# Optimization experiments

Measured on AMD Instinct MI355X. Metric: run time of the kernel, lower is better.

## Reference

```python
import jax, jax.numpy as jnp
import numpy as np

N, E, F_IN, D, R, L = 50000, 800000, 128, 64, 8, 3


def setup_inputs() -> dict:
    key = jax.random.key(0)
    ks = jax.random.split(key, 8)
    x = jax.random.normal(ks[0], (N, F_IN), dtype=jnp.float32)
    edge_index = jax.random.randint(ks[1], (2, E), 0, N)
    dist = jax.random.uniform(ks[2], (E,), dtype=jnp.float32)
    etype = jax.random.randint(ks[3], (E,), 0, R).astype(jnp.float32)
    edge_attr = jnp.stack([dist, etype], axis=1)  # [E, 2]: col0 distance, col1 relation id
    W_in = jax.random.normal(ks[4], (F_IN, D), dtype=jnp.float32) / np.float32(np.sqrt(F_IN))
    b_in = jnp.zeros((D,), jnp.float32)
    W_rel = jax.random.normal(ks[5], (L, R, D, D), dtype=jnp.float32) / np.float32(np.sqrt(D))
    W_root = jax.random.normal(ks[6], (L, D, D), dtype=jnp.float32) / np.float32(np.sqrt(D))
    b_conv = jnp.zeros((L, D), jnp.float32)
    return dict(x=x, edge_index=edge_index, edge_attr=edge_attr, W_in=W_in,
                b_in=b_in, W_rel=W_rel, W_root=W_root, b_conv=b_conv)


def rgcn_conv(h, src, dst, etype, Wr, Wroot, b):
    # PyG RGCNConv: per-relation MEAN aggregation + root weight + bias.
    # Composite segment id (dst, relation) -> one scatter over N*R segments.
    seg = dst * R + etype  # [E]
    msg = h[src]  # [E, D] gather
    s = jax.ops.segment_sum(msg, seg, num_segments=N * R)            # [N*R, D]
    cnt = jax.ops.segment_sum(jnp.ones((E,), h.dtype), seg, num_segments=N * R)
    mean = (s / jnp.maximum(cnt, 1.0)[:, None]).reshape(N, R, D)     # [N, R, D]
    return jnp.einsum('nrd,rde->ne', mean, Wr) + h @ Wroot + b


def reference(x, edge_index, edge_attr, W_in, b_in, W_rel, W_root, b_conv):
    edge_type = edge_attr[:, 1].astype(jnp.int32)
    edge_distance = edge_attr[:, 0]
    src, dst = edge_index[0], edge_index[1]
    h = jax.nn.relu(x @ W_in + b_in)
    for l in range(L):
        h = jax.nn.relu(rgcn_conv(h, src, dst, edge_type, W_rel[l], W_root[l], b_conv[l]))
    return h, edge_distance
```

## Files before the change

### kernel.cpp

```cpp
#include <hip/hip_runtime.h>

#define NN 50000
#define EE 800000
#define FIN 128
#define DD 64
#define RR 8
#define LL 3

#define ND (NN*DD)
#define NR (NN*RR)

#define SB 1024
#define NSB ((NR + SB - 1) / SB)
#define ECAP 2048
#define AS 72
#define KB 576

typedef __attribute__((ext_vector_type(8))) short bf16x8;
typedef __attribute__((ext_vector_type(4))) float f32x4;

__device__ __forceinline__ unsigned short f2bf(float x) {
  unsigned u = __float_as_uint(x);
  u += 0x7fff + ((u >> 16) & 1);
  return (unsigned short)(u >> 16);
}
__device__ __forceinline__ void split_bf(float x, short& h, short& l) {
  unsigned short hu = f2bf(x);
  float hf = __uint_as_float((unsigned)hu << 16);
  h = (short)hu;
  l = (short)f2bf(x - hf);
}

__global__ void k_prepB(const float* __restrict__ W_rel,
                        const float* __restrict__ W_root,
                        short* __restrict__ Btp) {
  const int idx = blockIdx.x * 256 + threadIdx.x;
  if (idx >= LL * DD * KB) return;
  const int k = idx % KB, n = (idx / KB) % DD, l = idx / (KB * DD);
  float w;
  if (k < 512) w = W_rel[(((size_t)l*RR + (k >> 6))*DD + (k & 63))*DD + n];
  else         w = W_root[((size_t)l*DD + (k - 512))*DD + n];
  short hi, lo; split_bf(w, hi, lo);
  Btp[((size_t)(l*2+0)*DD + n)*KB + k] = hi;
  Btp[((size_t)(l*2+1)*DD + n)*KB + k] = lo;
}
__global__ void k_prepWin(const float* __restrict__ W_in, short* __restrict__ Wt) {
  const int idx = blockIdx.x * 256 + threadIdx.x;
  if (idx >= DD * FIN) return;
  const int k = idx % FIN, n = idx / FIN;
  float w = W_in[(size_t)k*DD + n];
  short hi, lo; split_bf(w, hi, lo);
  Wt[((size_t)0*DD + n)*FIN + k] = hi;
  Wt[((size_t)1*DD + n)*FIN + k] = lo;
}

__global__ __launch_bounds__(256) void k_input_mfma(
    const float* __restrict__ x, const short* __restrict__ Wt,
    const float* __restrict__ b, float* __restrict__ h) {
  __shared__ short Ah[DD * 136];
  __shared__ short Al[DD * 136];
  const int t = threadIdx.x;
  const int lane = t & 63, wv = t >> 6;
  const int lr = lane & 15, lc = lane >> 4;
  const int n0 = blockIdx.x * 64;

  {
    const int row = t >> 2, cb = (t & 3) * 32;
    const int n = n0 + row;
    #pragma unroll
    for (int i = 0; i < 8; ++i) {
      const int col = cb + i * 4;
      float4 v = make_float4(0.f,0.f,0.f,0.f);
      if (n < NN) v = *(const float4*)(x + (size_t)n*FIN + col);
      short h0,l0,h1,l1,h2,l2,h3,l3;
      split_bf(v.x,h0,l0); split_bf(v.y,h1,l1);
      split_bf(v.z,h2,l2); split_bf(v.w,h3,l3);
      unsigned long long ph = (unsigned short)h0 | ((unsigned long long)(unsigned short)h1<<16)
          | ((unsigned long long)(unsigned short)h2<<32) | ((unsigned long long)(unsigned short)h3<<48);
      unsigned long long pl = (unsigned short)l0 | ((unsigned long long)(unsigned short)l1<<16)
          | ((unsigned long long)(unsigned short)l2<<32) | ((unsigned long long)(unsigned short)l3<<48);
      *(unsigned long long*)&Ah[row*136 + col] = ph;
      *(unsigned long long*)&Al[row*136 + col] = pl;
    }
  }
  __syncthreads();

  const int m0 = wv * 16;
  f32x4 acc[4];
  #pragma unroll
  for (int nt = 0; nt < 4; ++nt) acc[nt] = (f32x4){0.f,0.f,0.f,0.f};
  const int aoff = (m0 + lr)*136 + lc*8;
  int boff[4];
  #pragma unroll
  for (int nt = 0; nt < 4; ++nt) boff[nt] = (nt*16 + lr)*FIN + lc*8;

  #pragma unroll
  for (int ks = 0; ks < 4; ++ks) {
    const bf16x8 ah = *(const bf16x8*)&Ah[aoff + ks*32];
    const bf16x8 al = *(const bf16x8*)&Al[aoff + ks*32];
    #pragma unroll
    for (int nt = 0; nt < 4; ++nt) {
      const bf16x8 bh = *(const bf16x8*)(Wt + boff[nt] + ks*32);
      const bf16x8 bl = *(const bf16x8*)(Wt + DD*FIN + boff[nt] + ks*32);
      acc[nt] = __builtin_amdgcn_mfma_f32_16x16x32_bf16(ah, bh, acc[nt], 0, 0, 0);
      acc[nt] = __builtin_amdgcn_mfma_f32_16x16x32_bf16(al, bh, acc[nt], 0, 0, 0);
      acc[nt] = __builtin_amdgcn_mfma_f32_16x16x32_bf16(ah, bl, acc[nt], 0, 0, 0);
    }
  }
  #pragma unroll
  for (int nt = 0; nt < 4; ++nt) {
    const float bb = b[nt*16 + lr];
    #pragma unroll
    for (int i = 0; i < 4; ++i) {
      const int m = n0 + m0 + lc*4 + i;
      if (m < NN) h[(size_t)m*DD + nt*16 + lr] = fmaxf(acc[nt][i] + bb, 0.f);
    }
  }
}

__global__ void k_hist(const int* __restrict__ ei, const float* __restrict__ ea,
                       int* __restrict__ rp) {
  const int e = blockIdx.x * 256 + threadIdx.x;
  if (e >= EE) return;
  atomicAdd(&rp[(int)ea[2*e + 1] * NN + ei[EE + e]], 1);
}

__global__ __launch_bounds__(256) void k_scan1(int* __restrict__ rp,
                                               int* __restrict__ part) {
  __shared__ int ls[256];
  const int t = threadIdx.x;
  const int base = blockIdx.x * SB + t * 4;
  int v[4] = {0,0,0,0};
  #pragma unroll
  for (int i = 0; i < 4; ++i)
    if (base + i < NR) v[i] = rp[base + i];
  const int tsum = v[0] + v[1] + v[2] + v[3];
  ls[t] = tsum; __syncthreads();
  #pragma unroll
  for (int off = 1; off < 256; off <<= 1) {
    int x = (t >= off) ? ls[t - off] : 0;
    __syncthreads();
    ls[t] += x;
    __syncthreads();
  }
  if (t == 255) part[blockIdx.x] = ls[255];
  int run = ls[t] - tsum;
  #pragma unroll
  for (int i = 0; i < 4; ++i) {
    if (base + i < NR) rp[base + i] = run;
    run += v[i];
  }
}

__global__ __launch_bounds__(512) void k_scan2(int* __restrict__ part) {
  __shared__ int ls[512];
  const int t = threadIdx.x;
  const int v = (t < NSB) ? part[t] : 0;
  ls[t] = v; __syncthreads();
  #pragma unroll
  for (int off = 1; off < 512; off <<= 1) {
    int x = (t >= off) ? ls[t - off] : 0;
    __syncthreads();
    ls[t] += x;
    __syncthreads();
  }
  if (t < NSB) part[t] = ls[t] - v;
}

__global__ __launch_bounds__(256) void k_scan3(int* __restrict__ rp,
                                               const int* __restrict__ part,
                                               int* __restrict__ fill) {
  const int base = blockIdx.x * SB + threadIdx.x * 4;
  const int off = part[blockIdx.x];
  #pragma unroll
  for (int i = 0; i < 4; ++i)
    if (base + i < NR) {
      const int r = rp[base + i] + off;
      rp[base + i] = r;
      fill[base + i] = r;
    }
  if (blockIdx.x == 0 && threadIdx.x == 0) rp[NR] = EE;
}

__global__ void k_reorder(const int* __restrict__ ei, const float* __restrict__ ea,
                          int* __restrict__ fill, unsigned short* __restrict__ eidx) {
  const int e = blockIdx.x * 256 + threadIdx.x;
  if (e >= EE) return;
  const int key = (int)ea[2*e + 1] * NN + ei[EE + e];
  const int pos = atomicAdd(&fill[key], 1);
  eidx[pos] = (unsigned short)ei[e];
}

__global__ __launch_bounds__(256) void k_layer(
    const float* __restrict__ h, const unsigned short* __restrict__ eidx,
    const int* __restrict__ rp, const short* __restrict__ Btp,
    const float* __restrict__ bias, float* __restrict__ outh) {
  __shared__ short Ah[DD * AS];
  __shared__ short Al[DD * AS];
  __shared__ unsigned short els[ECAP];
  __shared__ int rpls[RR][65];
  __shared__ int baseL[RR + 1];

  const int t = threadIdx.x;
  const int lane = t & 63, wv = t >> 6;
  const int lr = lane & 15, lc = lane >> 4;
  const int n0 = blockIdx.x * 64;
  const int j0 = wv * 16;
  const float* hl = h + lane;

  for (int i = t; i < RR * 65; i += 256) {
    const int kk = i / 65, j = i - kk * 65;
    int g = n0 + j; if (g > NN) g = NN;
    rpls[kk][j] = rp[kk * NN + g];
  }
  __syncthreads();
  if (t == 0) {
    int s = 0;
    #pragma unroll
    for (int k = 0; k < RR; ++k) { baseL[k] = s; s += rpls[k][64] - rpls[k][0]; }
    baseL[RR] = s;
  }
  __syncthreads();
  const bool fit = baseL[RR] <= ECAP;
  if (fit) {
    for (int k = 0; k < RR; ++k) {
      const int g0 = rpls[k][0], sp = rpls[k][64] - g0, b0 = baseL[k];
      for (int i = t; i < sp; i += 256) els[b0 + i] = eidx[g0 + i];
    }
  }
  __syncthreads();

  auto gather = [&](int kk) {
    const int ebeg = rpls[kk][j0], eend = rpls[kk][j0 + 16];
    int j = j0;
    int nxt = rpls[kk][j0 + 1];
    float acc = 0.f;
    auto flush = [&]() {
      const int cnt = nxt - rpls[kk][j];
      float m = (cnt > 1) ? acc * (1.0f / (float)cnt) : acc;
      short hb, lb; split_bf(m, hb, lb);
      Ah[j * AS + lane] = hb;
      Al[j * AS + lane] = lb;
    };
    auto proc = [&](float v, int e2) {
      while (e2 >= nxt) { flush(); acc = 0.f; ++j; nxt = rpls[kk][j + 1]; }
      acc += v;
    };
    auto scan = [&](auto srcAt) {
      int e = ebeg;
      for (; e + 15 < eend; e += 16) {
        int s[16]; float v[16];
        #pragma unroll
        for (int i = 0; i < 16; ++i) s[i] = srcAt(e + i);
        #pragma unroll
        for (int i = 0; i < 16; ++i) v[i] = hl[(size_t)s[i] * DD];
        #pragma unroll
        for (int i = 0; i < 16; ++i) proc(v[i], e + i);
      }
      if (e + 7 < eend) {
        int s[8]; float v[8];
        #pragma unroll
        for (int i = 0; i < 8; ++i) s[i] = srcAt(e + i);
        #pragma unroll
        for (int i = 0; i < 8; ++i) v[i] = hl[(size_t)s[i] * DD];
        #pragma unroll
        for (int i = 0; i < 8; ++i) proc(v[i], e + i);
        e += 8;
      }
      for (; e < eend; ++e) proc(hl[(size_t)srcAt(e) * DD], e);
    };
    if (fit) {
      const int lb2 = baseL[kk] - rpls[kk][0];
      scan([&](int e) { return (int)els[lb2 + e]; });
    } else {
      scan([&](int e) { return (int)eidx[e]; });
    }
    while (true) {
      flush();
      acc = 0.f; ++j;
      if (j >= j0 + 16) break;
      nxt = rpls[kk][j + 1];
    }
  };
  auto root_stage = [&]() {
    for (int jj = 0; jj < 16; jj += 4) {
      float v[4];
      #pragma unroll
      for (int i = 0; i < 4; ++i) {
        const int n = n0 + j0 + jj + i;
        v[i] = (n < NN) ? h[(size_t)n * DD + lane] : 0.f;
      }
      #pragma unroll
      for (int i = 0; i < 4; ++i) {
        short hb, lb; split_bf(v[i], hb, lb);
        Ah[(j0 + jj + i) * AS + lane] = hb;
        Al[(j0 + jj + i) * AS + lane] = lb;
      }
    }
  };

  const int m0 = wv * 16;
  f32x4 acc[4];
  #pragma unroll
  for (int nt = 0; nt < 4; ++nt) acc[nt] = (f32x4){0.f,0.f,0.f,0.f};
  const int aoff = (m0 + lr) * AS + lc * 8;
  int boff[4];
  #pragma unroll
  for (int nt = 0; nt < 4; ++nt) boff[nt] = (nt*16 + lr)*KB + lc*8;
  const short* Blo = Btp + (size_t)DD * KB;

  #pragma unroll 1
  for (int kk = 0; kk < 9; ++kk) {
    if (kk < 8) gather(kk);
    else        root_stage();
    const int koff = kk * 64;
    #pragma unroll
    for (int ks = 0; ks < 2; ++ks) {
      const bf16x8 ah = *(const bf16x8*)&Ah[aoff + ks*32];
      const bf16x8 al = *(const bf16x8*)&Al[aoff + ks*32];
      #pragma unroll
      for (int nt = 0; nt < 4; ++nt) {
        const bf16x8 bh = *(const bf16x8*)(Btp + boff[nt] + koff + ks*32);
        const bf16x8 bl = *(const bf16x8*)(Blo + boff[nt] + koff + ks*32);
        acc[nt] = __builtin_amdgcn_mfma_f32_16x16x32_bf16(ah, bh, acc[nt], 0, 0, 0);
        acc[nt] = __builtin_amdgcn_mfma_f32_16x16x32_bf16(al, bh, acc[nt], 0, 0, 0);
        acc[nt] = __builtin_amdgcn_mfma_f32_16x16x32_bf16(ah, bl, acc[nt], 0, 0, 0);
      }
    }
  }

  #pragma unroll
  for (int nt = 0; nt < 4; ++nt) {
    const float bb = bias[nt*16 + lr];
    #pragma unroll
    for (int i = 0; i < 4; ++i) {
      const int m = n0 + m0 + lc*4 + i;
      if (m < NN) outh[(size_t)m*DD + nt*16 + lr] = fmaxf(acc[nt][i] + bb, 0.f);
    }
  }
}

__global__ void k_edist(const float* __restrict__ ea, float* __restrict__ out) {
  const int e = blockIdx.x * 256 + threadIdx.x;
  if (e < EE) out[e] = ea[2*e];
}

extern "C" void kernel_launch(void* const* d_in, const int* in_sizes, int n_in,
                              void* d_out, int out_size, void* d_ws, size_t ws_size,
                              hipStream_t stream) {
  const float* x      = (const float*)d_in[0];
  const int*   ei     = (const int*)d_in[1];
  const float* ea     = (const float*)d_in[2];
  const float* W_in   = (const float*)d_in[3];
  const float* b_in   = (const float*)d_in[4];
  const float* W_rel  = (const float*)d_in[5];
  const float* W_root = (const float*)d_in[6];
  const float* b_conv = (const float*)d_in[7];
  float* out = (float*)d_out;

  char* ws = (char*)d_ws;
  float*          hA   = (float*)(ws);
  float*          hB   = (float*)(ws + 12800000);
  int*            rp   = (int*)  (ws + 25600000);
  int*            fill = (int*)  (ws + 27200256);
  unsigned short* eidx = (unsigned short*)(ws + 28800256);
  int*            part = (int*)  (ws + 30400256);
  short*          Btp  = (short*)(ws + 30402304);
  short*          Wt   = (short*)(ws + 30844672);

  k_edist<<<(EE + 255)/256, 256, 0, stream>>>(ea, out + (size_t)ND);
  k_prepB<<<(LL*DD*KB + 255)/256, 256, 0, stream>>>(W_rel, W_root, Btp);
  k_prepWin<<<(DD*FIN + 255)/256, 256, 0, stream>>>(W_in, Wt);
  k_input_mfma<<<(NN + 63)/64, 256, 0, stream>>>(x, Wt, b_in, hA);

  hipMemsetAsync(rp, 0, (size_t)NR*4, stream);
  k_hist<<<(EE + 255)/256, 256, 0, stream>>>(ei, ea, rp);
  k_scan1<<<NSB, 256, 0, stream>>>(rp, part);
  k_scan2<<<1, 512, 0, stream>>>(part);
  k_scan3<<<NSB, 256, 0, stream>>>(rp, part, fill);
  k_reorder<<<(EE + 255)/256, 256, 0, stream>>>(ei, ea, fill, eidx);

  const int NBL = (NN + 63) / 64;
  const float* hin = hA;
  for (int l = 0; l < LL; ++l) {
    float* hout = (l == 2) ? out : ((l == 0) ? hB : hA);
    k_layer<<<NBL, 256, 0, stream>>>(hin, eidx, rp,
        Btp + (size_t)l*2*DD*KB, b_conv + (size_t)l*DD, hout);
    hin = hout;
  }
}
```

Measured before the change: 403.7 us.

## Software-pipeline edge gathers across relations and fuse small prep kernels

After: 796.6 us. 97.3% more time.

```diff
diff --git a/kernel.cpp b/kernel.cpp
--- a/kernel.cpp
+++ b/kernel.cpp
@@ -31,27 +31,27 @@
   l = (short)f2bf(x - hf);
 }
 
-__global__ void k_prepB(const float* __restrict__ W_rel,
-                        const float* __restrict__ W_root,
-                        short* __restrict__ Btp) {
+__global__ void k_prep(const float* __restrict__ W_rel,
+                       const float* __restrict__ W_root,
+                       const float* __restrict__ W_in,
+                       short* __restrict__ Btp, short* __restrict__ Wt) {
   const int idx = blockIdx.x * 256 + threadIdx.x;
-  if (idx >= LL * DD * KB) return;
-  const int k = idx % KB, n = (idx / KB) % DD, l = idx / (KB * DD);
-  float w;
-  if (k < 512) w = W_rel[(((size_t)l*RR + (k >> 6))*DD + (k & 63))*DD + n];
-  else         w = W_root[((size_t)l*DD + (k - 512))*DD + n];
-  short hi, lo; split_bf(w, hi, lo);
-  Btp[((size_t)(l*2+0)*DD + n)*KB + k] = hi;
-  Btp[((size_t)(l*2+1)*DD + n)*KB + k] = lo;
-}
-__global__ void k_prepWin(const float* __restrict__ W_in, short* __restrict__ Wt) {
-  const int idx = blockIdx.x * 256 + threadIdx.x;
-  if (idx >= DD * FIN) return;
-  const int k = idx % FIN, n = idx / FIN;
-  float w = W_in[(size_t)k*DD + n];
-  short hi, lo; split_bf(w, hi, lo);
-  Wt[((size_t)0*DD + n)*FIN + k] = hi;
-  Wt[((size_t)1*DD + n)*FIN + k] = lo;
+  if (idx < LL * DD * KB) {
+    const int k = idx % KB, n = (idx / KB) % DD, l = idx / (KB * DD);
+    float w;
+    if (k < 512) w = W_rel[(((size_t)l*RR + (k >> 6))*DD + (k & 63))*DD + n];
+    else         w = W_root[((size_t)l*DD + (k - 512))*DD + n];
+    short hi, lo; split_bf(w, hi, lo);
+    Btp[((size_t)(l*2+0)*DD + n)*KB + k] = hi;
+    Btp[((size_t)(l*2+1)*DD + n)*KB + k] = lo;
+  }
+  if (idx < DD * FIN) {
+    const int k = idx % FIN, n = idx / FIN;
+    float w = W_in[(size_t)k*DD + n];
+    short hi, lo; split_bf(w, hi, lo);
+    Wt[((size_t)0*DD + n)*FIN + k] = hi;
+    Wt[((size_t)1*DD + n)*FIN + k] = lo;
+  }
 }
 
 __global__ __launch_bounds__(256) void k_input_mfma(
@@ -119,10 +119,12 @@
 }
 
 __global__ void k_hist(const int* __restrict__ ei, const float* __restrict__ ea,
-                       int* __restrict__ rp) {
+                       int* __restrict__ rp, float* __restrict__ outd) {
   const int e = blockIdx.x * 256 + threadIdx.x;
   if (e >= EE) return;
-  atomicAdd(&rp[(int)ea[2*e + 1] * NN + ei[EE + e]], 1);
+  const float2 v = *(const float2*)(ea + 2*e);
+  outd[e] = v.x;
+  atomicAdd(&rp[(int)v.y * NN + ei[EE + e]], 1);
 }
 
 __global__ __launch_bounds__(256) void k_scan1(int* __restrict__ rp,
@@ -230,50 +232,71 @@
   }
   __syncthreads();
 
-  auto gather = [&](int kk) {
-    const int ebeg = rpls[kk][j0], eend = rpls[kk][j0 + 16];
-    int j = j0;
-    int nxt = rpls[kk][j0 + 1];
+  float va[16], vb[16];
+  auto issue16 = [&](float (&v)[16], int base, int ee1, int lb) {
+    #pragma unroll
+    for (int i = 0; i < 16; ++i) {
+      int idx = base + i;
+      idx = (idx < ee1) ? idx : ee1;
+      const int s = fit ? (int)els[lb + idx] : (int)eidx[idx];
+      v[i] = hl[(size_t)s * DD];
+    }
+  };
+
+  const int m0 = wv * 16;
+  f32x4 acc4[4];
+  #pragma unroll
+  for (int nt = 0; nt < 4; ++nt) acc4[nt] = (f32x4){0.f,0.f,0.f,0.f};
+  const int aoff = (m0 + lr) * AS + lc * 8;
+  int boff[4];
+  #pragma unroll
+  for (int nt = 0; nt < 4; ++nt) boff[nt] = (nt*16 + lr)*KB + lc*8;
+  const short* Blo = Btp + (size_t)DD * KB;
+
+  {
+    const int eb = rpls[0][j0], ee = rpls[0][j0 + 16];
+    const int lb = fit ? (baseL[0] - rpls[0][0]) : 0;
+    if (eb < ee) {
+      issue16(va, eb, ee - 1, lb);
+      if (eb + 16 < ee) issue16(vb, eb + 16, ee - 1, lb);
+    }
+  }
+
+  #pragma unroll 1
+  for (int kk = 0; kk < 8; ++kk) {
+    const int eb = rpls[kk][j0], ee = rpls[kk][j0 + 16];
+    const int lb = fit ? (baseL[kk] - rpls[kk][0]) : 0;
+    int j = j0, nxt = rpls[kk][j0 + 1];
     float acc = 0.f;
     auto flush = [&]() {
       const int cnt = nxt - rpls[kk][j];
       float m = (cnt > 1) ? acc * (1.0f / (float)cnt) : acc;
-      short hb, lb; split_bf(m, hb, lb);
+      short hb, lbv; split_bf(m, hb, lbv);
       Ah[j * AS + lane] = hb;
-      Al[j * AS + lane] = lb;
+      Al[j * AS + lane] = lbv;
     };
     auto proc = [&](float v, int e2) {
       while (e2 >= nxt) { flush(); acc = 0.f; ++j; nxt = rpls[kk][j + 1]; }
       acc += v;
     };
-    auto scan = [&](auto srcAt) {
-      int e = ebeg;
-      for (; e + 15 < eend; e += 16) {
-        int s[16]; float v[16];
-        #pragma unroll
-        for (int i = 0; i < 16; ++i) s[i] = srcAt(e + i);
-        #pragma unroll
-        for (int i = 0; i < 16; ++i) v[i] = hl[(size_t)s[i] * DD];
-        #pragma unroll
-        for (int i = 0; i < 16; ++i) proc(v[i], e + i);
+    auto procB = [&](float (&v)[16], int base) {
+      #pragma unroll
+      for (int i = 0; i < 16; ++i)
+        if (base + i < ee) proc(v[i], base + i);
+    };
+
+    if (eb < ee) {
+      int base = eb;
+      while (true) {
+        if (base + 16 >= ee) { procB(va, base); break; }
+        procB(va, base);
+        if (base + 32 < ee) issue16(va, base + 32, ee - 1, lb);
+        base += 16;
+        if (base + 16 >= ee) { procB(vb, base); break; }
+        procB(vb, base);
+        if (base + 32 < ee) issue16(vb, base + 32, ee - 1, lb);
+        base += 16;
       }
-      if (e + 7 < eend) {
-        int s[8]; float v[8];
-        #pragma unroll
-        for (int i = 0; i < 8; ++i) s[i] = srcAt(e + i);
-        #pragma unroll
-        for (int i = 0; i < 8; ++i) v[i] = hl[(size_t)s[i] * DD];
-        #pragma unroll
-        for (int i = 0; i < 8; ++i) proc(v[i], e + i);
-        e += 8;
-      }
-      for (; e < eend; ++e) proc(hl[(size_t)srcAt(e) * DD], e);
-    };
-    if (fit) {
-      const int lb2 = baseL[kk] - rpls[kk][0];
-      scan([&](int e) { return (int)els[lb2 + e]; });
-    } else {
-      scan([&](int e) { return (int)eidx[e]; });
     }
     while (true) {
       flush();
@@ -281,38 +304,22 @@
       if (j >= j0 + 16) break;
       nxt = rpls[kk][j + 1];
     }
-  };
-  auto root_stage = [&]() {
-    for (int jj = 0; jj < 16; jj += 4) {
-      float v[4];
+
+    if (kk < 7) {
+      const int eb2 = rpls[kk + 1][j0], ee2 = rpls[kk + 1][j0 + 16];
+      const int lbn = fit ? (baseL[kk + 1] - rpls[kk + 1][0]) : 0;
+      if (eb2 < ee2) {
+        issue16(va, eb2, ee2 - 1, lbn);
+        if (eb2 + 16 < ee2) issue16(vb, eb2 + 16, ee2 - 1, lbn);
+      }
+    } else {
       #pragma unroll
-      for (int i = 0; i < 4; ++i) {
-        const int n = n0 + j0 + jj + i;
-        v[i] = (n < NN) ? h[(size_t)n * DD + lane] : 0.f;
+      for (int i = 0; i < 16; ++i) {
+        const int n = n0 + j0 + i;
+        va[i] = (n < NN) ? h[(size_t)n * DD + lane] : 0.f;
       }
-      #pragma unroll
-      for (int i = 0; i < 4; ++i) {
-        short hb, lb; split_bf(v[i], hb, lb);
-        Ah[(j0 + jj + i) * AS + lane] = hb;
-        Al[(j0 + jj + i) * AS + lane] = lb;
-      }
-    }
-  };
-
-  const int m0 = wv * 16;
-  f32x4 acc[4];
-  #pragma unroll
-  for (int nt = 0; nt < 4; ++nt) acc[nt] = (f32x4){0.f,0.f,0.f,0.f};
-  const int aoff = (m0 + lr) * AS + lc * 8;
-  int boff[4];
-  #pragma unroll
-  for (int nt = 0; nt < 4; ++nt) boff[nt] = (nt*16 + lr)*KB + lc*8;
-  const short* Blo = Btp + (size_t)DD * KB;
-
-  #pragma unroll 1
-  for (int kk = 0; kk < 9; ++kk) {
-    if (kk < 8) gather(kk);
-    else        root_stage();
+    }
+
     const int koff = kk * 64;
     #pragma unroll
     for (int ks = 0; ks < 2; ++ks) {
@@ -322,9 +329,32 @@
       for (int nt = 0; nt < 4; ++nt) {
         const bf16x8 bh = *(const bf16x8*)(Btp + boff[nt] + koff + ks*32);
         const bf16x8 bl = *(const bf16x8*)(Blo + boff[nt] + koff + ks*32);
-        acc[nt] = __builtin_amdgcn_mfma_f32_16x16x32_bf16(ah, bh, acc[nt], 0, 0, 0);
-        acc[nt] = __builtin_amdgcn_mfma_f32_16x16x32_bf16(al, bh, acc[nt], 0, 0, 0);
-        acc[nt] = __builtin_amdgcn_mfma_f32_16x16x32_bf16(ah, bl, acc[nt], 0, 0, 0);
+        acc4[nt] = __builtin_amdgcn_mfma_f32_16x16x32_bf16(ah, bh, acc4[nt], 0, 0, 0);
+        acc4[nt] = __builtin_amdgcn_mfma_f32_16x16x32_bf16(al, bh, acc4[nt], 0, 0, 0);
+        acc4[nt] = __builtin_amdgcn_mfma_f32_16x16x32_bf16(ah, bl, acc4[nt], 0, 0, 0);
+      }
+    }
+  }
+
+  #pragma unroll
+  for (int i = 0; i < 16; ++i) {
+    short hb, lbv; split_bf(va[i], hb, lbv);
+    Ah[(j0 + i) * AS + lane] = hb;
+    Al[(j0 + i) * AS + lane] = lbv;
+  }
+  {
+    const int koff = 512;
+    #pragma unroll
+    for (int ks = 0; ks < 2; ++ks) {
+      const bf16x8 ah = *(const bf16x8*)&Ah[aoff + ks*32];
+      const bf16x8 al = *(const bf16x8*)&Al[aoff + ks*32];
+      #pragma unroll
+      for (int nt = 0; nt < 4; ++nt) {
+        const bf16x8 bh = *(const bf16x8*)(Btp + boff[nt] + koff + ks*32);
+        const bf16x8 bl = *(const bf16x8*)(Blo + boff[nt] + koff + ks*32);
+        acc4[nt] = __builtin_amdgcn_mfma_f32_16x16x32_bf16(ah, bh, acc4[nt], 0, 0, 0);
+        acc4[nt] = __builtin_amdgcn_mfma_f32_16x16x32_bf16(al, bh, acc4[nt], 0, 0, 0);
+        acc4[nt] = __builtin_amdgcn_mfma_f32_16x16x32_bf16(ah, bl, acc4[nt], 0, 0, 0);
       }
     }
   }
@@ -335,14 +365,9 @@
     #pragma unroll
     for (int i = 0; i < 4; ++i) {
       const int m = n0 + m0 + lc*4 + i;
-      if (m < NN) outh[(size_t)m*DD + nt*16 + lr] = fmaxf(acc[nt][i] + bb, 0.f);
-    }
-  }
-}
-
-__global__ void k_edist(const float* __restrict__ ea, float* __restrict__ out) {
-  const int e = blockIdx.x * 256 + threadIdx.x;
-  if (e < EE) out[e] = ea[2*e];
+      if (m < NN) outh[(size_t)m*DD + nt*16 + lr] = fmaxf(acc4[nt][i] + bb, 0.f);
+    }
+  }
 }
 
 extern "C" void kernel_launch(void* const* d_in, const int* in_sizes, int n_in,
@@ -368,13 +393,11 @@
   short*          Btp  = (short*)(ws + 30402304);
   short*          Wt   = (short*)(ws + 30844672);
 
-  k_edist<<<(EE + 255)/256, 256, 0, stream>>>(ea, out + (size_t)ND);
-  k_prepB<<<(LL*DD*KB + 255)/256, 256, 0, stream>>>(W_rel, W_root, Btp);
-  k_prepWin<<<(DD*FIN + 255)/256, 256, 0, stream>>>(W_in, Wt);
+  k_prep<<<(LL*DD*KB + 255)/256, 256, 0, stream>>>(W_rel, W_root, W_in, Btp, Wt);
   k_input_mfma<<<(NN + 63)/64, 256, 0, stream>>>(x, Wt, b_in, hA);
 
   hipMemsetAsync(rp, 0, (size_t)NR*4, stream);
-  k_hist<<<(EE + 255)/256, 256, 0, stream>>>(ei, ea, rp);
+  k_hist<<<(EE + 255)/256, 256, 0, stream>>>(ei, ea, rp, out + (size_t)ND);
   k_scan1<<<NSB, 256, 0, stream>>>(rp, part);
   k_scan2<<<1, 512, 0, stream>>>(part);
   k_scan3<<<NSB, 256, 0, stream>>>(rp, part, fill);
```

## Split relation gather across wave pairs with split-K reduction in layer kernel

Applied to the files above, without the earlier changes.

New measurement: 455.3 us. +12.8%, slower.

```diff
diff --git a/kernel.cpp b/kernel.cpp
--- a/kernel.cpp
+++ b/kernel.cpp
@@ -12,8 +12,8 @@
 
 #define SB 1024
 #define NSB ((NR + SB - 1) / SB)
-#define ECAP 2048
-#define AS 72
+#define ECAP 1024
+#define ASF 68
 #define KB 576
 
 typedef __attribute__((ext_vector_type(8))) short bf16x8;
@@ -31,27 +31,27 @@
   l = (short)f2bf(x - hf);
 }
 
-__global__ void k_prepB(const float* __restrict__ W_rel,
-                        const float* __restrict__ W_root,
-                        short* __restrict__ Btp) {
+__global__ void k_prep(const float* __restrict__ W_rel,
+                       const float* __restrict__ W_root,
+                       const float* __restrict__ W_in,
+                       short* __restrict__ Btp, short* __restrict__ Wt) {
   const int idx = blockIdx.x * 256 + threadIdx.x;
-  if (idx >= LL * DD * KB) return;
-  const int k = idx % KB, n = (idx / KB) % DD, l = idx / (KB * DD);
-  float w;
-  if (k < 512) w = W_rel[(((size_t)l*RR + (k >> 6))*DD + (k & 63))*DD + n];
-  else         w = W_root[((size_t)l*DD + (k - 512))*DD + n];
-  short hi, lo; split_bf(w, hi, lo);
-  Btp[((size_t)(l*2+0)*DD + n)*KB + k] = hi;
-  Btp[((size_t)(l*2+1)*DD + n)*KB + k] = lo;
-}
-__global__ void k_prepWin(const float* __restrict__ W_in, short* __restrict__ Wt) {
-  const int idx = blockIdx.x * 256 + threadIdx.x;
-  if (idx >= DD * FIN) return;
-  const int k = idx % FIN, n = idx / FIN;
-  float w = W_in[(size_t)k*DD + n];
-  short hi, lo; split_bf(w, hi, lo);
-  Wt[((size_t)0*DD + n)*FIN + k] = hi;
-  Wt[((size_t)1*DD + n)*FIN + k] = lo;
+  if (idx < LL * DD * KB) {
+    const int k = idx % KB, n = (idx / KB) % DD, l = idx / (KB * DD);
+    float w;
+    if (k < 512) w = W_rel[(((size_t)l*RR + (k >> 6))*DD + (k & 63))*DD + n];
+    else         w = W_root[((size_t)l*DD + (k - 512))*DD + n];
+    short hi, lo; split_bf(w, hi, lo);
+    Btp[((size_t)(l*2+0)*DD + n)*KB + k] = hi;
+    Btp[((size_t)(l*2+1)*DD + n)*KB + k] = lo;
+  }
+  if (idx < DD * FIN) {
+    const int k = idx % FIN, n = idx / FIN;
+    float w = W_in[(size_t)k*DD + n];
+    short hi, lo; split_bf(w, hi, lo);
+    Wt[((size_t)0*DD + n)*FIN + k] = hi;
+    Wt[((size_t)1*DD + n)*FIN + k] = lo;
+  }
 }
 
 __global__ __launch_bounds__(256) void k_input_mfma(
@@ -119,10 +119,12 @@
 }
 
 __global__ void k_hist(const int* __restrict__ ei, const float* __restrict__ ea,
-                       int* __restrict__ rp) {
+                       int* __restrict__ rp, float* __restrict__ outd) {
   const int e = blockIdx.x * 256 + threadIdx.x;
   if (e >= EE) return;
-  atomicAdd(&rp[(int)ea[2*e + 1] * NN + ei[EE + e]], 1);
+  const float2 v = *(const float2*)(ea + 2*e);
+  outd[e] = v.x;
+  atomicAdd(&rp[(int)v.y * NN + ei[EE + e]], 1);
 }
 
 __global__ __launch_bounds__(256) void k_scan1(int* __restrict__ rp,
@@ -191,25 +193,25 @@
   eidx[pos] = (unsigned short)ei[e];
 }
 
-__global__ __launch_bounds__(256) void k_layer(
+__global__ __launch_bounds__(256, 6) void k_layer(
     const float* __restrict__ h, const unsigned short* __restrict__ eidx,
     const int* __restrict__ rp, const short* __restrict__ Btp,
     const float* __restrict__ bias, float* __restrict__ outh) {
-  __shared__ short Ah[DD * AS];
-  __shared__ short Al[DD * AS];
+  __shared__ float Af[4][16 * ASF];
   __shared__ unsigned short els[ECAP];
-  __shared__ int rpls[RR][65];
+  __shared__ int rpls[RR][33];
   __shared__ int baseL[RR + 1];
 
   const int t = threadIdx.x;
   const int lane = t & 63, wv = t >> 6;
+  const int pair = wv >> 1, half = wv & 1;
   const int lr = lane & 15, lc = lane >> 4;
-  const int n0 = blockIdx.x * 64;
-  const int j0 = wv * 16;
+  const int n0 = blockIdx.x * 32;
+  const int j0 = pair * 16;
   const float* hl = h + lane;
 
-  for (int i = t; i < RR * 65; i += 256) {
-    const int kk = i / 65, j = i - kk * 65;
+  for (int i = t; i < RR * 33; i += 256) {
+    const int kk = i / 33, j = i - kk * 33;
     int g = n0 + j; if (g > NN) g = NN;
     rpls[kk][j] = rp[kk * NN + g];
   }
@@ -217,18 +219,20 @@
   if (t == 0) {
     int s = 0;
     #pragma unroll
-    for (int k = 0; k < RR; ++k) { baseL[k] = s; s += rpls[k][64] - rpls[k][0]; }
+    for (int k = 0; k < RR; ++k) { baseL[k] = s; s += rpls[k][32] - rpls[k][0]; }
     baseL[RR] = s;
   }
   __syncthreads();
   const bool fit = baseL[RR] <= ECAP;
   if (fit) {
     for (int k = 0; k < RR; ++k) {
-      const int g0 = rpls[k][0], sp = rpls[k][64] - g0, b0 = baseL[k];
+      const int g0 = rpls[k][0], sp = rpls[k][32] - g0, b0 = baseL[k];
       for (int i = t; i < sp; i += 256) els[b0 + i] = eidx[g0 + i];
     }
   }
   __syncthreads();
+
+  float* Aw = Af[wv];
 
   auto gather = [&](int kk) {
     const int ebeg = rpls[kk][j0], eend = rpls[kk][j0 + 16];
@@ -238,9 +242,7 @@
     auto flush = [&]() {
       const int cnt = nxt - rpls[kk][j];
       float m = (cnt > 1) ? acc * (1.0f / (float)cnt) : acc;
-      short hb, lb; split_bf(m, hb, lb);
-      Ah[j * AS + lane] = hb;
-      Al[j * AS + lane] = lb;
+      Aw[(j - j0) * ASF + lane] = m;
     };
     auto proc = [&](float v, int e2) {
       while (e2 >= nxt) { flush(); acc = 0.f; ++j; nxt = rpls[kk][j + 1]; }
@@ -291,58 +293,73 @@
         v[i] = (n < NN) ? h[(size_t)n * DD + lane] : 0.f;
       }
       #pragma unroll
-      for (int i = 0; i < 4; ++i) {
-        short hb, lb; split_bf(v[i], hb, lb);
-        Ah[(j0 + jj + i) * AS + lane] = hb;
-        Al[(j0 + jj + i) * AS + lane] = lb;
-      }
+      for (int i = 0; i < 4; ++i) Aw[(jj + i) * ASF + lane] = v[i];
     }
   };
 
-  const int m0 = wv * 16;
-  f32x4 acc[4];
-  #pragma unroll
-  for (int nt = 0; nt < 4; ++nt) acc[nt] = (f32x4){0.f,0.f,0.f,0.f};
-  const int aoff = (m0 + lr) * AS + lc * 8;
+  f32x4 acc4[4];
+  #pragma unroll
+  for (int nt = 0; nt < 4; ++nt) acc4[nt] = (f32x4){0.f,0.f,0.f,0.f};
   int boff[4];
   #pragma unroll
   for (int nt = 0; nt < 4; ++nt) boff[nt] = (nt*16 + lr)*KB + lc*8;
   const short* Blo = Btp + (size_t)DD * KB;
-
-  #pragma unroll 1
-  for (int kk = 0; kk < 9; ++kk) {
-    if (kk < 8) gather(kk);
-    else        root_stage();
-    const int koff = kk * 64;
+  const float* arow = Aw + lr * ASF + lc * 8;
+
+  auto mfma_slice = [&](int koff) {
     #pragma unroll
     for (int ks = 0; ks < 2; ++ks) {
-      const bf16x8 ah = *(const bf16x8*)&Ah[aoff + ks*32];
-      const bf16x8 al = *(const bf16x8*)&Al[aoff + ks*32];
+      const f32x4 a0 = *(const f32x4*)(arow + ks*32);
+      const f32x4 a1 = *(const f32x4*)(arow + ks*32 + 4);
+      bf16x8 ah, al;
+      #pragma unroll
+      for (int i = 0; i < 4; ++i) {
+        short hb, lb;
+        split_bf(a0[i], hb, lb); ah[i] = hb;     al[i] = lb;
+        split_bf(a1[i], hb, lb); ah[4 + i] = hb; al[4 + i] = lb;
+      }
       #pragma unroll
       for (int nt = 0; nt < 4; ++nt) {
         const bf16x8 bh = *(const bf16x8*)(Btp + boff[nt] + koff + ks*32);
         const bf16x8 bl = *(const bf16x8*)(Blo + boff[nt] + koff + ks*32);
-        acc[nt] = __builtin_amdgcn_mfma_f32_16x16x32_bf16(ah, bh, acc[nt], 0, 0, 0);
-        acc[nt] = __builtin_amdgcn_mfma_f32_16x16x32_bf16(al, bh, acc[nt], 0, 0, 0);
-        acc[nt] = __builtin_amdgcn_mfma_f32_16x16x32_bf16(ah, bl, acc[nt], 0, 0, 0);
-      }
-    }
-  }
-
-  #pragma unroll
-  for (int nt = 0; nt < 4; ++nt) {
-    const float bb = bias[nt*16 + lr];
-    #pragma unroll
-    for (int i = 0; i < 4; ++i) {
-      const int m = n0 + m0 + lc*4 + i;
-      if (m < NN) outh[(size_t)m*DD + nt*16 + lr] = fmaxf(acc[nt][i] + bb, 0.f);
-    }
-  }
-}
-
-__global__ void k_edist(const float* __restrict__ ea, float* __restrict__ out) {
-  const int e = blockIdx.x * 256 + threadIdx.x;
-  if (e < EE) out[e] = ea[2*e];
+        acc4[nt] = __builtin_amdgcn_mfma_f32_16x16x32_bf16(ah, bh, acc4[nt], 0, 0, 0);
+        acc4[nt] = __builtin_amdgcn_mfma_f32_16x16x32_bf16(al, bh, acc4[nt], 0, 0, 0);
+        acc4[nt] = __builtin_amdgcn_mfma_f32_16x16x32_bf16(ah, bl, acc4[nt], 0, 0, 0);
+      }
+    }
+  };
+
+  #pragma unroll 1
+  for (int kx = 0; kx < 4; ++kx) {
+    const int kk = half * 4 + kx;
+    gather(kk);
+    mfma_slice(kk * 64);
+  }
+  if (!half) {
+    root_stage();
+    mfma_slice(512);
+  } else {
+    #pragma unroll
+    for (int nt = 0; nt < 4; ++nt)
+      #pragma unroll
+      for (int i = 0; i < 4; ++i)
+        Aw[(lc*4 + i) * ASF + nt*16 + lr] = acc4[nt][i];
+  }
+  __syncthreads();
+  if (!half) {
+    const float* Pw = Af[wv + 1];
+    #pragma unroll
+    for (int nt = 0; nt < 4; ++nt) {
+      const float bb = bias[nt*16 + lr];
+      #pragma unroll
+      for (int i = 0; i < 4; ++i) {
+        const int m = n0 + j0 + lc*4 + i;
+        if (m < NN)
+          outh[(size_t)m*DD + nt*16 + lr] =
+              fmaxf(acc4[nt][i] + Pw[(lc*4 + i) * ASF + nt*16 + lr] + bb, 0.f);
+      }
+    }
+  }
 }
 
 extern "C" void kernel_launch(void* const* d_in, const int* in_sizes, int n_in,
@@ -368,19 +385,17 @@
   short*          Btp  = (short*)(ws + 30402304);
   short*          Wt   = (short*)(ws + 30844672);
 
-  k_edist<<<(EE + 255)/256, 256, 0, stream>>>(ea, out + (size_t)ND);
-  k_prepB<<<(LL*DD*KB + 255)/256, 256, 0, stream>>>(W_rel, W_root, Btp);
-  k_prepWin<<<(DD*FIN + 255)/256, 256, 0, stream>>>(W_in, Wt);
+  k_prep<<<(LL*DD*KB + 255)/256, 256, 0, stream>>>(W_rel, W_root, W_in, Btp, Wt);
   k_input_mfma<<<(NN + 63)/64, 256, 0, stream>>>(x, Wt, b_in, hA);
 
   hipMemsetAsync(rp, 0, (size_t)NR*4, stream);
-  k_hist<<<(EE + 255)/256, 256, 0, stream>>>(ei, ea, rp);
+  k_hist<<<(EE + 255)/256, 256, 0, stream>>>(ei, ea, rp, out + (size_t)ND);
   k_scan1<<<NSB, 256, 0, stream>>>(rp, part);
   k_scan2<<<1, 512, 0, stream>>>(part);
   k_scan3<<<NSB, 256, 0, stream>>>(rp, part, fill);
   k_reorder<<<(EE + 255)/256, 256, 0, stream>>>(ei, ea, fill, eidx);
 
-  const int NBL = (NN + 63) / 64;
+  const int NBL = (NN + 31) / 32;
   const float* hin = hA;
   for (int l = 0; l < LL; ++l) {
     float* hout = (l == 2) ? out : ((l == 0) ? hB : hA);
```
